# Kernel optimization log

Hardware: AMD Instinct MI355X
Metric: run time of the kernel (lower is better)

## Reference

```python
import jax, jax.numpy as jnp
import numpy as np

NUM_HEADS = 16
D_MODEL = 1024
NEG_INF = -1e30


def setup_inputs() -> dict:
    key = jax.random.key(0)
    ks = jax.random.split(key, 7)
    B, S, D = 2, 2048, D_MODEL
    scale = 1.0 / np.sqrt(D)
    return {
        "queries": jax.random.normal(ks[0], (B, S, D), dtype=jnp.float32),
        "keys": jax.random.normal(ks[1], (B, S, D), dtype=jnp.float32),
        "values": jax.random.normal(ks[2], (B, S, D), dtype=jnp.float32),
        "Wq": jax.random.normal(ks[3], (D, D), dtype=jnp.float32) * scale,
        "Wk": jax.random.normal(ks[4], (D, D), dtype=jnp.float32) * scale,
        "Wv": jax.random.normal(ks[5], (D, D), dtype=jnp.float32) * scale,
        "Wo": jax.random.normal(ks[6], (D, D), dtype=jnp.float32) * scale,
    }


def _split_heads(x, h):
    # [B, S, D] -> [B, h, S, D/h]
    B, S, D = x.shape
    return x.reshape(B, S, h, D // h).transpose(0, 2, 1, 3)


def reference(queries, keys, values, Wq, Wk, Wv, Wo):
    h = NUM_HEADS
    q = _split_heads(queries @ Wq, h)  # [B, h, S, dh]
    k = _split_heads(keys @ Wk, h)
    v = _split_heads(values @ Wv, h)
    dh = q.shape[-1]
    scores = jnp.einsum("bhqd,bhkd->bhqk", q, k) / jnp.sqrt(jnp.float32(dh))
    # original quirk: exactly-zero scores are masked to -1e30 before softmax
    scores = jnp.where(scores == 0, NEG_INF, scores)
    attn = jax.nn.softmax(scores, axis=-1)
    out = jnp.einsum("bhqk,bhkd->bhqd", attn, v)  # [B, h, S, dh]
    B, _, S, _ = out.shape
    out = out.transpose(0, 2, 1, 3).reshape(B, S, h * dh)
    return out @ Wo
```

## Files before the change

kernel.cpp:

```cpp
#include <hip/hip_runtime.h>

typedef unsigned short u16;
typedef short bf16x8 __attribute__((ext_vector_type(8)));
typedef float f32x4 __attribute__((ext_vector_type(4)));
typedef float f32x16 __attribute__((ext_vector_type(16)));

namespace {

constexpr int kB = 2, kS = 2048, kD = 1024, kH = 16, kDh = 64;
constexpr float kC2 = 0.125f * 1.44269504088896341f;

__device__ inline u16 f32_bf16(float f) {
    unsigned u = __float_as_uint(f);
    u += 0x7FFFu + ((u >> 16) & 1u);
    return (u16)(u >> 16);
}

__device__ inline u16 f32_bf16_fast(float f) {
    return (u16)((__float_as_uint(f) + 0x8000u) >> 16);
}

__device__ inline float fast_exp2(float x) {
    float r;
    asm("v_exp_f32 %0, %1" : "=v"(r) : "v"(x));
    return r;
}

__device__ inline void gl_lds16(const void* g, void* l) {
    __builtin_amdgcn_global_load_lds(
        (const __attribute__((address_space(1))) void*)g,
        (__attribute__((address_space(3))) void*)l, 16, 0, 0);
}

__device__ inline int swz8(int l) {
    return ((l & 3) ^ ((l >> 2) & 3) ^ ((l >> 4) & 3)) * 8;
}

__global__ __launch_bounds__(256) void conv_bf16_3(
    const float* __restrict__ s0, const float* __restrict__ s1,
    const float* __restrict__ s2,
    u16* __restrict__ d0, u16* __restrict__ d1, u16* __restrict__ d2)
{
    const int z = blockIdx.y;
    const float* src = z == 0 ? s0 : (z == 1 ? s1 : s2);
    u16* dst = z == 0 ? d0 : (z == 1 ? d1 : d2);
    const int i = blockIdx.x * 256 + threadIdx.x;
    const float4* s4 = (const float4*)src;
    float4 a = s4[2 * i], b = s4[2 * i + 1];
    uint4 o;
    o.x = (unsigned)f32_bf16(a.x) | ((unsigned)f32_bf16(a.y) << 16);
    o.y = (unsigned)f32_bf16(a.z) | ((unsigned)f32_bf16(a.w) << 16);
    o.z = (unsigned)f32_bf16(b.x) | ((unsigned)f32_bf16(b.y) << 16);
    o.w = (unsigned)f32_bf16(b.z) | ((unsigned)f32_bf16(b.w) << 16);
    ((uint4*)dst)[i] = o;
}

__global__ __launch_bounds__(256) void wtrans4(
    const float* __restrict__ W0, const float* __restrict__ W1,
    const float* __restrict__ W2, const float* __restrict__ W3,
    u16* __restrict__ T0, u16* __restrict__ T1,
    u16* __restrict__ T2, u16* __restrict__ T3)
{
    const int z = blockIdx.z;
    const float* W = z == 0 ? W0 : (z == 1 ? W1 : (z == 2 ? W2 : W3));
    u16* Wt = z == 0 ? T0 : (z == 1 ? T1 : (z == 2 ? T2 : T3));
    const float sc = (z == 0) ? kC2 : 1.0f;

    __shared__ __attribute__((aligned(16))) u16 T[64][65];
    const int t = threadIdx.x;
    const int n0 = blockIdx.x * 64, k0 = blockIdx.y * 64;
    const int r = t >> 4, c4 = (t & 15) * 4;
#pragma unroll
    for (int it = 0; it < 4; ++it) {
        const int rr = r + 16 * it;
        float4 v = *(const float4*)(W + (size_t)(k0 + rr) * kD + n0 + c4);
        T[rr][c4 + 0] = f32_bf16(v.x * sc);
        T[rr][c4 + 1] = f32_bf16(v.y * sc);
        T[rr][c4 + 2] = f32_bf16(v.z * sc);
        T[rr][c4 + 3] = f32_bf16(v.w * sc);
    }
    __syncthreads();
#pragma unroll
    for (int it = 0; it < 4; ++it) {
        const int nn = r + 16 * it;
        uint2 pk;
        pk.x = (unsigned)T[c4 + 0][nn] | ((unsigned)T[c4 + 1][nn] << 16);
        pk.y = (unsigned)T[c4 + 2][nn] | ((unsigned)T[c4 + 3][nn] << 16);
        *(uint2*)(Wt + (size_t)(n0 + nn) * kD + k0 + c4) = pk;
    }
}

__global__ __launch_bounds__(256) void vtrans(
    const u16* __restrict__ V, u16* __restrict__ Vt)
{
    __shared__ __attribute__((aligned(16))) u16 T[64][65];
    const int t = threadIdx.x;
    const int s0 = blockIdx.x * 64;
    const int bh = blockIdx.y, b = bh >> 4, h = bh & 15;
    const int rr = t >> 3, c0 = (t & 7) * 8;
    union { u16 u[8]; uint4 v4; } buf;
#pragma unroll
    for (int p = 0; p < 2; ++p) {
        const int s = rr + 32 * p;
        buf.v4 = *(const uint4*)(V + (size_t)(b * kS + s0 + s) * kD + h * kDh + c0);
#pragma unroll
        for (int i = 0; i < 8; ++i) T[c0 + i][s] = buf.u[i];
    }
    __syncthreads();
#pragma unroll
    for (int p = 0; p < 2; ++p) {
        const int d = rr + 32 * p;
#pragma unroll
        for (int i = 0; i < 8; ++i) buf.u[i] = T[d][c0 + i];
        *(uint4*)(Vt + (size_t)(bh * kDh + d) * kS + s0 + c0) = buf.v4;
    }
}

template <bool F32OUT>
__device__ inline void gemm128_body(
    const u16* __restrict__ A, const u16* __restrict__ Wt,
    void* __restrict__ Cout, int M, int N, int K, int bx, int by)
{
    __shared__ __attribute__((aligned(16))) u16 As[128 * 32];
    __shared__ __attribute__((aligned(16))) u16 Bs[128 * 32];
    const int t = threadIdx.x, w = t >> 6, l = t & 63;
    const int quad = l >> 4, c = l & 15;
    const int wm = w >> 1, wn = w & 1;
    const int m0 = by * 128, n0 = bx * 128;
    const int lr = l >> 2, lc = swz8(l);
    const int xc = ((quad ^ (c & 3) ^ ((c >> 2) & 3))) * 8;

    const u16* ga0 = A  + (size_t)(m0 + w * 32 + lr) * K + lc;
    const u16* ga1 = A  + (size_t)(m0 + w * 32 + 16 + lr) * K + lc;
    const u16* gb0 = Wt + (size_t)(n0 + w * 32 + lr) * K + lc;
    const u16* gb1 = Wt + (size_t)(n0 + w * 32 + 16 + lr) * K + lc;
    u16* la0 = &As[(w * 32) * 32];
    u16* la1 = &As[(w * 32 + 16) * 32];
    u16* lb0 = &Bs[(w * 32) * 32];
    u16* lb1 = &Bs[(w * 32 + 16) * 32];

    f32x4 acc[4][4];
#pragma unroll
    for (int mi = 0; mi < 4; ++mi)
#pragma unroll
        for (int nj = 0; nj < 4; ++nj) acc[mi][nj] = 0;

    for (int k0 = 0; k0 < K; k0 += 32) {
        gl_lds16(ga0 + k0, la0);
        gl_lds16(ga1 + k0, la1);
        gl_lds16(gb0 + k0, lb0);
        gl_lds16(gb1 + k0, lb1);
        __syncthreads();
        bf16x8 af[4], bf[4];
#pragma unroll
        for (int mi = 0; mi < 4; ++mi)
            af[mi] = *(const bf16x8*)&As[(wm * 64 + mi * 16 + c) * 32 + xc];
#pragma unroll
        for (int nj = 0; nj < 4; ++nj)
            bf[nj] = *(const bf16x8*)&Bs[(wn * 64 + nj * 16 + c) * 32 + xc];
#pragma unroll
        for (int mi = 0; mi < 4; ++mi)
#pragma unroll
            for (int nj = 0; nj < 4; ++nj)
                acc[mi][nj] = __builtin_amdgcn_mfma_f32_16x16x32_bf16(
                    af[mi], bf[nj], acc[mi][nj], 0, 0, 0);
        __syncthreads();
    }

#pragma unroll
    for (int mi = 0; mi < 4; ++mi)
#pragma unroll
        for (int nj = 0; nj < 4; ++nj)
#pragma unroll
            for (int r = 0; r < 4; ++r) {
                const size_t row = m0 + wm * 64 + mi * 16 + quad * 4 + r;
                const size_t col = n0 + wn * 64 + nj * 16 + c;
                if (F32OUT)
                    ((float*)Cout)[row * N + col] = acc[mi][nj][r];
                else
                    ((u16*)Cout)[row * N + col] = f32_bf16(acc[mi][nj][r]);
            }
}

__global__ __launch_bounds__(256) void gemm_qkv(
    const u16* __restrict__ A0, const u16* __restrict__ A1,
    const u16* __restrict__ A2,
    const u16* __restrict__ W0, const u16* __restrict__ W1,
    const u16* __restrict__ W2,
    u16* __restrict__ C0, u16* __restrict__ C1, u16* __restrict__ C2)
{
    const int z = blockIdx.z;
    const u16* A  = z == 0 ? A0 : (z == 1 ? A1 : A2);
    const u16* Wt = z == 0 ? W0 : (z == 1 ? W1 : W2);
    u16* C = z == 0 ? C0 : (z == 1 ? C1 : C2);
    gemm128_body<false>(A, Wt, C, kB * kS, kD, kD, blockIdx.x, blockIdx.y);
}

__global__ __launch_bounds__(256) void gemm_out(
    const u16* __restrict__ A, const u16* __restrict__ Wt,
    float* __restrict__ C)
{
    __shared__ __attribute__((aligned(16))) u16 As[64 * 32];
    __shared__ __attribute__((aligned(16))) u16 Bs[128 * 32];
    const int N = kD, K = kD;
    const int t = threadIdx.x, w = t >> 6, l = t & 63;
    const int quad = l >> 4, c = l & 15;
    const int wm = w >> 1, wn = w & 1;
    const int m0 = blockIdx.y * 64, n0 = blockIdx.x * 128;
    const int lr = l >> 2, lc = swz8(l);
    const int xc = ((quad ^ (c & 3) ^ ((c >> 2) & 3))) * 8;

    const u16* ga  = A  + (size_t)(m0 + w * 16 + lr) * K + lc;
    const u16* gb0 = Wt + (size_t)(n0 + w * 16 + lr) * K + lc;
    const u16* gb1 = Wt + (size_t)(n0 + 64 + w * 16 + lr) * K + lc;
    u16* la  = &As[(w * 16) * 32];
    u16* lb0 = &Bs[(w * 16) * 32];
    u16* lb1 = &Bs[(64 + w * 16) * 32];

    f32x4 acc[2][4];
#pragma unroll
    for (int mi = 0; mi < 2; ++mi)
#pragma unroll
        for (int nj = 0; nj < 4; ++nj) acc[mi][nj] = 0;

    for (int k0 = 0; k0 < K; k0 += 32) {
        gl_lds16(ga + k0, la);
        gl_lds16(gb0 + k0, lb0);
        gl_lds16(gb1 + k0, lb1);
        __syncthreads();
        bf16x8 af[2], bf[4];
#pragma unroll
        for (int mi = 0; mi < 2; ++mi)
            af[mi] = *(const bf16x8*)&As[(wm * 32 + mi * 16 + c) * 32 + xc];
#pragma unroll
        for (int nj = 0; nj < 4; ++nj)
            bf[nj] = *(const bf16x8*)&Bs[(wn * 64 + nj * 16 + c) * 32 + xc];
#pragma unroll
        for (int mi = 0; mi < 2; ++mi)
#pragma unroll
            for (int nj = 0; nj < 4; ++nj)
                acc[mi][nj] = __builtin_amdgcn_mfma_f32_16x16x32_bf16(
                    af[mi], bf[nj], acc[mi][nj], 0, 0, 0);
        __syncthreads();
    }

#pragma unroll
    for (int mi = 0; mi < 2; ++mi)
#pragma unroll
        for (int nj = 0; nj < 4; ++nj)
#pragma unroll
            for (int r = 0; r < 4; ++r) {
                const size_t row = m0 + wm * 32 + mi * 16 + quad * 4 + r;
                const size_t col = n0 + wn * 64 + nj * 16 + c;
                C[row * N + col] = acc[mi][nj][r];
            }
}

__global__ __launch_bounds__(256) void attn(
    const u16* __restrict__ Q, const u16* __restrict__ K,
    const u16* __restrict__ Vt, u16* __restrict__ AO)
{
    __shared__ __attribute__((aligned(16))) u16 KsL[2][64 * 64];
    __shared__ __attribute__((aligned(16))) u16 VtL[2][64 * 64];
    __shared__ __attribute__((aligned(16))) u16 QPs[4 * 32 * 64];

    const int t = threadIdx.x, w = t >> 6, l = t & 63;
    const int half = l >> 5, m = l & 31;
    const int q0 = blockIdx.x * 128;
    const int bh = blockIdx.y, b = bh >> 4, h = bh & 15;
    const int sl = l >> 3;
    const int sc = (l & 7) ^ sl;

    const size_t kbase = (size_t)(b * kS) * kD + h * kDh;
    const size_t vbase = (size_t)bh * kDh * kS;

    const size_t qbase = (size_t)(b * kS + q0 + w * 32) * kD + h * kDh;
#pragma unroll
    for (int i = 0; i < 4; ++i)
        gl_lds16(Q + qbase + (size_t)(i * 8 + sl) * kD + sc * 8,
                 &QPs[w * 2048 + i * 512]);
#pragma unroll
    for (int i = 0; i < 2; ++i) {
        const int R0 = w * 16 + i * 8;
        gl_lds16(K + kbase + (size_t)(R0 + sl) * kD + sc * 8, &KsL[0][R0 * 64]);
        gl_lds16(Vt + vbase + (size_t)(R0 + sl) * kS + sc * 8, &VtL[0][R0 * 64]);
    }
    __syncthreads();

    bf16x8 qf[4];
#pragma unroll
    for (int ch = 0; ch < 4; ++ch)
        qf[ch] = *(const bf16x8*)
            &QPs[w * 2048 + m * 64 + ((2 * ch + half) ^ (m & 7)) * 8];

    bf16x8 ones;
#pragma unroll
    for (int i = 0; i < 8; ++i) ones[i] = (short)0x3F80;

    f32x16 o0 = 0, o1 = 0, ol = 0;

    for (int kt = 0; kt < kS / 64; ++kt) {
        const int cur = kt & 1;

        if (kt + 1 < kS / 64) {
#pragma unroll
            for (int i = 0; i < 2; ++i) {
                const int R0 = w * 16 + i * 8;
                gl_lds16(K + kbase + (size_t)((kt + 1) * 64 + R0 + sl) * kD + sc * 8,
                         &KsL[cur ^ 1][R0 * 64]);
                gl_lds16(Vt + vbase + (size_t)(R0 + sl) * kS + (kt + 1) * 64 + sc * 8,
                         &VtL[cur ^ 1][R0 * 64]);
            }
        }

        f32x16 s0 = 0, s1 = 0;
#pragma unroll
        for (int ch = 0; ch < 4; ++ch) {
            const int xo = ((2 * ch + half) ^ (m & 7)) * 8;
            const bf16x8 kf0 = *(const bf16x8*)&KsL[cur][(m) * 64 + xo];
            const bf16x8 kf1 = *(const bf16x8*)&KsL[cur][(32 + m) * 64 + xo];
            s0 = __builtin_amdgcn_mfma_f32_32x32x16_bf16(qf[ch], kf0, s0, 0, 0, 0);
            s1 = __builtin_amdgcn_mfma_f32_32x32x16_bf16(qf[ch], kf1, s1, 0, 0, 0);
        }

#pragma unroll
        for (int reg = 0; reg < 16; ++reg) {
            const int qrow = (reg & 3) + 8 * (reg >> 2) + 4 * half;
            const int base = w * 2048 + qrow * 64;
            const int sw = (qrow & 7);
            {
                const int key = m;
                QPs[base + ((key >> 3) ^ sw) * 8 + (key & 7)] =
                    f32_bf16_fast(fast_exp2(s0[reg]));
            }
            {
                const int key = 32 + m;
                QPs[base + ((key >> 3) ^ sw) * 8 + (key & 7)] =
                    f32_bf16_fast(fast_exp2(s1[reg]));
            }
        }

#pragma unroll
        for (int ch = 0; ch < 4; ++ch) {
            const int xo = ((2 * ch + half) ^ (m & 7)) * 8;
            const bf16x8 pf = *(const bf16x8*)&QPs[w * 2048 + m * 64 + xo];
            const bf16x8 vf0 = *(const bf16x8*)&VtL[cur][(m) * 64 + xo];
            const bf16x8 vf1 = *(const bf16x8*)&VtL[cur][(32 + m) * 64 + xo];
            o0 = __builtin_amdgcn_mfma_f32_32x32x16_bf16(pf, vf0, o0, 0, 0, 0);
            o1 = __builtin_amdgcn_mfma_f32_32x32x16_bf16(pf, vf1, o1, 0, 0, 0);
            ol = __builtin_amdgcn_mfma_f32_32x32x16_bf16(pf, ones, ol, 0, 0, 0);
        }
        __syncthreads();
    }

    const size_t obase = (size_t)(b * kS + q0 + w * 32) * kD + h * kDh;
#pragma unroll
    for (int reg = 0; reg < 16; ++reg) {
        const int qrow = (reg & 3) + 8 * (reg >> 2) + 4 * half;
        const float inv = 1.0f / ol[reg];
        AO[obase + (size_t)qrow * kD + m]      = f32_bf16(o0[reg] * inv);
        AO[obase + (size_t)qrow * kD + 32 + m] = f32_bf16(o1[reg] * inv);
    }
}

}

extern "C" void kernel_launch(void* const* d_in, const int* in_sizes, int n_in,
                              void* d_out, int out_size, void* d_ws, size_t ws_size,
                              hipStream_t stream)
{
    const float* q_in = (const float*)d_in[0];
    const float* k_in = (const float*)d_in[1];
    const float* v_in = (const float*)d_in[2];
    const float* Wq   = (const float*)d_in[3];
    const float* Wk   = (const float*)d_in[4];
    const float* Wv   = (const float*)d_in[5];
    const float* Wo   = (const float*)d_in[6];

    u16* ws = (u16*)d_ws;
    const size_t M1 = 1u << 20;
    u16* xq  = ws;
    u16* xk  = ws + 4 * M1;
    u16* xv  = ws + 8 * M1;
    u16* Wtq = ws + 12 * M1;
    u16* Wtk = ws + 13 * M1;
    u16* Wtv = ws + 14 * M1;
    u16* Wto = ws + 15 * M1;
    u16* Qp  = ws + 16 * M1;
    u16* Kp  = ws + 20 * M1;
    u16* Vp  = ws + 24 * M1;
    u16* AO  = ws + 28 * M1;
    u16* Vtg = xq;

    hipLaunchKernelGGL(conv_bf16_3, dim3(2048, 3), dim3(256), 0, stream,
                       q_in, k_in, v_in, xq, xk, xv);

    hipLaunchKernelGGL(wtrans4, dim3(16, 16, 4), dim3(256), 0, stream,
                       Wq, Wk, Wv, Wo, Wtq, Wtk, Wtv, Wto);

    hipLaunchKernelGGL(gemm_qkv, dim3(8, 32, 3), dim3(256), 0, stream,
                       xq, xk, xv, Wtq, Wtk, Wtv, Qp, Kp, Vp);

    hipLaunchKernelGGL(vtrans, dim3(32, 32), dim3(256), 0, stream, Vp, Vtg);

    hipLaunchKernelGGL(attn, dim3(16, 32), dim3(256), 0, stream, Qp, Kp, Vtg, AO);

    hipLaunchKernelGGL(gemm_out, dim3(8, 64), dim3(256), 0, stream,
                       AO, Wto, (float*)d_out);
}
```

Measured before the change: 242.1 us.

## Merge prep kernels and switch attention to register-staged single LDS buffer

Fuses the activation bf16 conversion and weight transpose kernels into one launch, with a 2D grid where the extra rows handle the transposes and the surplus blocks exit early. In the attention kernel, the double-buffered direct global-to-LDS loads are replaced by prefetching the next K/V tile into registers, then writing it into a single LDS buffer between two barriers. This halves K/V LDS use, which may allow more resident blocks, and removes one launch. The cost is an extra barrier per tile, more registers, and an exposed LDS write phase. The prep launch also creates many blocks that immediately return.

```diff
diff --git a/kernel.cpp b/kernel.cpp
--- a/kernel.cpp
+++ b/kernel.cpp
@@ -36,39 +36,39 @@
     return ((l & 3) ^ ((l >> 2) & 3) ^ ((l >> 4) & 3)) * 8;
 }
 
-__global__ __launch_bounds__(256) void conv_bf16_3(
+__global__ __launch_bounds__(256) void prep(
     const float* __restrict__ s0, const float* __restrict__ s1,
     const float* __restrict__ s2,
-    u16* __restrict__ d0, u16* __restrict__ d1, u16* __restrict__ d2)
-{
-    const int z = blockIdx.y;
-    const float* src = z == 0 ? s0 : (z == 1 ? s1 : s2);
-    u16* dst = z == 0 ? d0 : (z == 1 ? d1 : d2);
-    const int i = blockIdx.x * 256 + threadIdx.x;
-    const float4* s4 = (const float4*)src;
-    float4 a = s4[2 * i], b = s4[2 * i + 1];
-    uint4 o;
-    o.x = (unsigned)f32_bf16(a.x) | ((unsigned)f32_bf16(a.y) << 16);
-    o.y = (unsigned)f32_bf16(a.z) | ((unsigned)f32_bf16(a.w) << 16);
-    o.z = (unsigned)f32_bf16(b.x) | ((unsigned)f32_bf16(b.y) << 16);
-    o.w = (unsigned)f32_bf16(b.z) | ((unsigned)f32_bf16(b.w) << 16);
-    ((uint4*)dst)[i] = o;
-}
-
-__global__ __launch_bounds__(256) void wtrans4(
+    u16* __restrict__ d0, u16* __restrict__ d1, u16* __restrict__ d2,
     const float* __restrict__ W0, const float* __restrict__ W1,
     const float* __restrict__ W2, const float* __restrict__ W3,
     u16* __restrict__ T0, u16* __restrict__ T1,
     u16* __restrict__ T2, u16* __restrict__ T3)
 {
-    const int z = blockIdx.z;
+    const int y = blockIdx.y;
+    if (y < 3) {
+        const float* src = y == 0 ? s0 : (y == 1 ? s1 : s2);
+        u16* dst = y == 0 ? d0 : (y == 1 ? d1 : d2);
+        const int i = blockIdx.x * 256 + threadIdx.x;
+        const float4* s4 = (const float4*)src;
+        float4 a = s4[2 * i], b = s4[2 * i + 1];
+        uint4 o;
+        o.x = (unsigned)f32_bf16(a.x) | ((unsigned)f32_bf16(a.y) << 16);
+        o.y = (unsigned)f32_bf16(a.z) | ((unsigned)f32_bf16(a.w) << 16);
+        o.z = (unsigned)f32_bf16(b.x) | ((unsigned)f32_bf16(b.y) << 16);
+        o.w = (unsigned)f32_bf16(b.z) | ((unsigned)f32_bf16(b.w) << 16);
+        ((uint4*)dst)[i] = o;
+        return;
+    }
+    if (blockIdx.x >= 256) return;
+    const int z = y - 3;
     const float* W = z == 0 ? W0 : (z == 1 ? W1 : (z == 2 ? W2 : W3));
     u16* Wt = z == 0 ? T0 : (z == 1 ? T1 : (z == 2 ? T2 : T3));
     const float sc = (z == 0) ? kC2 : 1.0f;
 
     __shared__ __attribute__((aligned(16))) u16 T[64][65];
     const int t = threadIdx.x;
-    const int n0 = blockIdx.x * 64, k0 = blockIdx.y * 64;
+    const int n0 = (blockIdx.x & 15) * 64, k0 = (blockIdx.x >> 4) * 64;
     const int r = t >> 4, c4 = (t & 15) * 4;
 #pragma unroll
     for (int it = 0; it < 4; ++it) {
@@ -260,8 +260,8 @@
     const u16* __restrict__ Q, const u16* __restrict__ K,
     const u16* __restrict__ Vt, u16* __restrict__ AO)
 {
-    __shared__ __attribute__((aligned(16))) u16 KsL[2][64 * 64];
-    __shared__ __attribute__((aligned(16))) u16 VtL[2][64 * 64];
+    __shared__ __attribute__((aligned(16))) u16 KsL[64 * 64];
+    __shared__ __attribute__((aligned(16))) u16 VtL[64 * 64];
     __shared__ __attribute__((aligned(16))) u16 QPs[4 * 32 * 64];
 
     const int t = threadIdx.x, w = t >> 6, l = t & 63;
@@ -270,20 +270,28 @@
     const int bh = blockIdx.y, b = bh >> 4, h = bh & 15;
     const int sl = l >> 3;
     const int sc = (l & 7) ^ sl;
+    const int cc = l & 7;
+    const int R0w = w * 16;
 
     const size_t kbase = (size_t)(b * kS) * kD + h * kDh;
     const size_t vbase = (size_t)bh * kDh * kS;
-
     const size_t qbase = (size_t)(b * kS + q0 + w * 32) * kD + h * kDh;
+
 #pragma unroll
     for (int i = 0; i < 4; ++i)
         gl_lds16(Q + qbase + (size_t)(i * 8 + sl) * kD + sc * 8,
                  &QPs[w * 2048 + i * 512]);
+
+    uint4 kreg[2], vreg[2];
 #pragma unroll
     for (int i = 0; i < 2; ++i) {
-        const int R0 = w * 16 + i * 8;
-        gl_lds16(K + kbase + (size_t)(R0 + sl) * kD + sc * 8, &KsL[0][R0 * 64]);
-        gl_lds16(Vt + vbase + (size_t)(R0 + sl) * kS + sc * 8, &VtL[0][R0 * 64]);
+        kreg[i] = *(const uint4*)(K + kbase + (size_t)(R0w + i * 8 + sl) * kD + sc * 8);
+        vreg[i] = *(const uint4*)(Vt + vbase + (size_t)(R0w + i * 8 + sl) * kS + sc * 8);
+    }
+#pragma unroll
+    for (int i = 0; i < 2; ++i) {
+        *(uint4*)&KsL[(R0w + i * 8 + sl) * 64 + cc * 8] = kreg[i];
+        *(uint4*)&VtL[(R0w + i * 8 + sl) * 64 + cc * 8] = vreg[i];
     }
     __syncthreads();
 
@@ -298,18 +306,16 @@
     for (int i = 0; i < 8; ++i) ones[i] = (short)0x3F80;
 
     f32x16 o0 = 0, o1 = 0, ol = 0;
-
-    for (int kt = 0; kt < kS / 64; ++kt) {
-        const int cur = kt & 1;
-
-        if (kt + 1 < kS / 64) {
+    constexpr int NT = kS / 64;
+
+    for (int kt = 0; kt < NT; ++kt) {
+        if (kt + 1 < NT) {
 #pragma unroll
             for (int i = 0; i < 2; ++i) {
-                const int R0 = w * 16 + i * 8;
-                gl_lds16(K + kbase + (size_t)((kt + 1) * 64 + R0 + sl) * kD + sc * 8,
-                         &KsL[cur ^ 1][R0 * 64]);
-                gl_lds16(Vt + vbase + (size_t)(R0 + sl) * kS + (kt + 1) * 64 + sc * 8,
-                         &VtL[cur ^ 1][R0 * 64]);
+                kreg[i] = *(const uint4*)
+                    (K + kbase + (size_t)((kt + 1) * 64 + R0w + i * 8 + sl) * kD + sc * 8);
+                vreg[i] = *(const uint4*)
+                    (Vt + vbase + (size_t)(R0w + i * 8 + sl) * kS + (kt + 1) * 64 + sc * 8);
             }
         }
 
@@ -317,8 +323,8 @@
 #pragma unroll
         for (int ch = 0; ch < 4; ++ch) {
             const int xo = ((2 * ch + half) ^ (m & 7)) * 8;
-            const bf16x8 kf0 = *(const bf16x8*)&KsL[cur][(m) * 64 + xo];
-            const bf16x8 kf1 = *(const bf16x8*)&KsL[cur][(32 + m) * 64 + xo];
+            const bf16x8 kf0 = *(const bf16x8*)&KsL[(m) * 64 + xo];
+            const bf16x8 kf1 = *(const bf16x8*)&KsL[(32 + m) * 64 + xo];
             s0 = __builtin_amdgcn_mfma_f32_32x32x16_bf16(qf[ch], kf0, s0, 0, 0, 0);
             s1 = __builtin_amdgcn_mfma_f32_32x32x16_bf16(qf[ch], kf1, s1, 0, 0, 0);
         }
@@ -344,13 +350,22 @@
         for (int ch = 0; ch < 4; ++ch) {
             const int xo = ((2 * ch + half) ^ (m & 7)) * 8;
             const bf16x8 pf = *(const bf16x8*)&QPs[w * 2048 + m * 64 + xo];
-            const bf16x8 vf0 = *(const bf16x8*)&VtL[cur][(m) * 64 + xo];
-            const bf16x8 vf1 = *(const bf16x8*)&VtL[cur][(32 + m) * 64 + xo];
+            const bf16x8 vf0 = *(const bf16x8*)&VtL[(m) * 64 + xo];
+            const bf16x8 vf1 = *(const bf16x8*)&VtL[(32 + m) * 64 + xo];
             o0 = __builtin_amdgcn_mfma_f32_32x32x16_bf16(pf, vf0, o0, 0, 0, 0);
             o1 = __builtin_amdgcn_mfma_f32_32x32x16_bf16(pf, vf1, o1, 0, 0, 0);
             ol = __builtin_amdgcn_mfma_f32_32x32x16_bf16(pf, ones, ol, 0, 0, 0);
         }
-        __syncthreads();
+
+        if (kt + 1 < NT) {
+            __syncthreads();
+#pragma unroll
+            for (int i = 0; i < 2; ++i) {
+                *(uint4*)&KsL[(R0w + i * 8 + sl) * 64 + cc * 8] = kreg[i];
+                *(uint4*)&VtL[(R0w + i * 8 + sl) * 64 + cc * 8] = vreg[i];
+            }
+            __syncthreads();
+        }
     }
 
     const size_t obase = (size_t)(b * kS + q0 + w * 32) * kD + h * kDh;
@@ -392,10 +407,8 @@
     u16* AO  = ws + 28 * M1;
     u16* Vtg = xq;
 
-    hipLaunchKernelGGL(conv_bf16_3, dim3(2048, 3), dim3(256), 0, stream,
-                       q_in, k_in, v_in, xq, xk, xv);
-
-    hipLaunchKernelGGL(wtrans4, dim3(16, 16, 4), dim3(256), 0, stream,
+    hipLaunchKernelGGL(prep, dim3(2048, 7), dim3(256), 0, stream,
+                       q_in, k_in, v_in, xq, xk, xv,
                        Wq, Wk, Wv, Wo, Wtq, Wtk, Wtv, Wto);
 
     hipLaunchKernelGGL(gemm_qkv, dim3(8, 32, 3), dim3(256), 0, stream,
```

Result: slower. 252.6 us (+4.4%).
